# Optimization experiments

Measured on AMD Instinct MI355X. Metric: run time of the kernel, lower is better.

Reference implementation:

```python
import jax, jax.numpy as jnp
import numpy as np

U, M, E, EL, H, F, C = 200000, 100000, 2000000, 500000, 64, 20, 7


def setup_inputs() -> dict:
    key = jax.random.key(0)
    ks = jax.random.split(key, 20)
    s = 0.02
    return {
        "user_node_id": jnp.arange(U, dtype=jnp.int64),
        "movie_node_id": jnp.arange(M, dtype=jnp.int64),
        "movie_x": jax.random.normal(ks[0], (M, F), jnp.float32),
        "edge_src": jax.random.randint(ks[1], (E,), 0, U),
        "edge_dst": jax.random.randint(ks[2], (E,), 0, M),
        "el_src": jax.random.randint(ks[3], (EL,), 0, U),
        "el_dst": jax.random.randint(ks[4], (EL,), 0, M),
        "user_emb": jax.random.normal(ks[5], (U, H), jnp.float32) * s,
        "movie_emb": jax.random.normal(ks[6], (M, H), jnp.float32) * s,
        "w_movie": jax.random.normal(ks[7], (F, H), jnp.float32) * s,
        "b_movie": jnp.zeros((H,), jnp.float32),
        "l1_rates_Wl": jax.random.normal(ks[8], (H, H), jnp.float32) * s,
        "l1_rates_bl": jnp.zeros((H,), jnp.float32),
        "l1_rates_Wr": jax.random.normal(ks[9], (H, H), jnp.float32) * s,
        "l1_rev_Wl": jax.random.normal(ks[10], (H, H), jnp.float32) * s,
        "l1_rev_bl": jnp.zeros((H,), jnp.float32),
        "l1_rev_Wr": jax.random.normal(ks[11], (H, H), jnp.float32) * s,
        "l2_rates_Wl": jax.random.normal(ks[12], (H, H), jnp.float32) * s,
        "l2_rates_bl": jnp.zeros((H,), jnp.float32),
        "l2_rates_Wr": jax.random.normal(ks[13], (H, H), jnp.float32) * s,
        "l2_rev_Wl": jax.random.normal(ks[14], (H, H), jnp.float32) * s,
        "l2_rev_bl": jnp.zeros((H,), jnp.float32),
        "l2_rev_Wr": jax.random.normal(ks[15], (H, H), jnp.float32) * s,
        "cls_W": jax.random.normal(ks[16], (2 * H, C), jnp.float32) * s,
        "cls_b": jnp.zeros((C,), jnp.float32),
    }


def _sage(x_src, x_dst, src, dst, n_dst, Wl, bl, Wr):
    # mean-aggregate neighbor messages: gather -> segment_sum -> divide by degree
    msg = x_src[src]                                            # [E, H]
    agg = jax.ops.segment_sum(msg, dst, num_segments=n_dst)     # [n_dst, H]
    deg = jax.ops.segment_sum(jnp.ones((src.shape[0],), x_src.dtype), dst,
                              num_segments=n_dst)
    agg = agg / jnp.maximum(deg, 1.0)[:, None]
    return agg @ Wl + bl + x_dst @ Wr                           # SAGEConv: lin_l(aggr) + lin_r(root)


def reference(user_node_id, movie_node_id, movie_x, edge_src, edge_dst,
              el_src, el_dst, user_emb, movie_emb, w_movie, b_movie,
              l1_rates_Wl, l1_rates_bl, l1_rates_Wr,
              l1_rev_Wl, l1_rev_bl, l1_rev_Wr,
              l2_rates_Wl, l2_rates_bl, l2_rates_Wr,
              l2_rev_Wl, l2_rev_bl, l2_rev_Wr,
              cls_W, cls_b):
    # input projections
    x_user = user_emb[user_node_id]                              # [U, H]
    x_movie = movie_x @ w_movie + b_movie + movie_emb[movie_node_id]  # [M, H]

    # hetero GNN layer 1 (relu)
    u1 = jax.nn.relu(_sage(x_movie, x_user, edge_dst, edge_src, x_user.shape[0],
                           l1_rev_Wl, l1_rev_bl, l1_rev_Wr))
    m1 = jax.nn.relu(_sage(x_user, x_movie, edge_src, edge_dst, x_movie.shape[0],
                           l1_rates_Wl, l1_rates_bl, l1_rates_Wr))
    # hetero GNN layer 2 (no activation)
    u2 = _sage(m1, u1, edge_dst, edge_src, u1.shape[0],
               l2_rev_Wl, l2_rev_bl, l2_rev_Wr)
    m2 = _sage(u1, m1, edge_src, edge_dst, m1.shape[0],
               l2_rates_Wl, l2_rates_bl, l2_rates_Wr)

    # edge classifier over labeled (user, movie) pairs
    edge_feat = jnp.concatenate([u2[el_src], m2[el_dst]], axis=-1)  # [EL, 2H]
    return edge_feat @ cls_W + cls_b                                # [EL, C]
```

## Files before the change

kernel.cpp:

```cpp
#include <hip/hip_runtime.h>
#include <cstdint>
#include <cstddef>

#define H 64
#define C 7
#define F 20
#define BSH 9
#define BSZ 512
#define CH 8192

typedef unsigned short u16;
typedef __attribute__((ext_vector_type(8))) short bf16x8;
typedef __attribute__((ext_vector_type(4))) float f32x4;
typedef __attribute__((ext_vector_type(2))) float f32x2;

static __device__ __forceinline__ int imax(int a, int b) { return a > b ? a : b; }
static __device__ __forceinline__ int imin(int a, int b) { return a < b ? a : b; }

static __device__ __forceinline__ float bf2f(u16 v) {
  union { unsigned u; float f; } x; x.u = ((unsigned)v) << 16; return x.f;
}
static __device__ __forceinline__ u16 f2bf(float f) {
  union { float f; unsigned u; } x; x.f = f;
  unsigned r = x.u + 0x7fffu + ((x.u >> 16) & 1u);
  return (u16)(r >> 16);
}
static __device__ __forceinline__ int pack2bf(float a, float b) {
  return (int)f2bf(a) | ((int)f2bf(b) << 16);
}
static __device__ __forceinline__ float lo16f(unsigned v) {
  union { unsigned u; float f; } x; x.u = v << 16; return x.f;
}
static __device__ __forceinline__ float hi16f(unsigned v) {
  union { unsigned u; float f; } x; x.u = v & 0xffff0000u; return x.f;
}
static __device__ __forceinline__ int cvtpk_bf16(float a, float b) {
  int w;
  asm("v_cvt_pk_bf16_f32 %0, %1, %2" : "=v"(w) : "v"(a), "v"(b));
  return w;
}

__global__ __launch_bounds__(256) void k_bhist(const int* __restrict__ esrc,
                                               const int* __restrict__ edst, int E,
                                               int* __restrict__ gcnt_u, int* __restrict__ gcnt_m,
                                               int nbu, int nbm) {
  extern __shared__ int sh[];
  int* hu = sh;
  int* hm = sh + nbu;
  for (int i = threadIdx.x; i < nbu + nbm; i += 256) sh[i] = 0;
  __syncthreads();
  int stride = gridDim.x * 256;
  for (int i = blockIdx.x * 256 + threadIdx.x; i < E; i += stride) {
    atomicAdd(&hu[esrc[i] >> BSH], 1);
    atomicAdd(&hm[edst[i] >> BSH], 1);
  }
  __syncthreads();
  for (int i = threadIdx.x; i < nbu; i += 256) if (hu[i]) atomicAdd(&gcnt_u[i], hu[i]);
  for (int i = threadIdx.x; i < nbm; i += 256) if (hm[i]) atomicAdd(&gcnt_m[i], hm[i]);
}

__global__ __launch_bounds__(256) void k_bscan(const int* __restrict__ gcnt_u,
                                               const int* __restrict__ gcnt_m,
                                               int nbu, int nbm, int E,
                                               int* __restrict__ boff_u, int* __restrict__ boff_m,
                                               int* __restrict__ gcur_u, int* __restrict__ gcur_m) {
  __shared__ int s[1024];
  for (int i = threadIdx.x; i < nbu; i += 256) s[i] = gcnt_u[i];
  for (int i = threadIdx.x; i < nbm; i += 256) s[512 + i] = gcnt_m[i];
  __syncthreads();
  if (threadIdx.x == 0) {
    int r = 0;
    for (int i = 0; i < nbu; ++i) { int v = s[i]; s[i] = r; r += v; }
  }
  if (threadIdx.x == 1) {
    int r = 0;
    for (int i = 0; i < nbm; ++i) { int v = s[512 + i]; s[512 + i] = r; r += v; }
  }
  __syncthreads();
  for (int i = threadIdx.x; i < nbu; i += 256) { boff_u[i] = s[i]; gcur_u[i] = s[i]; }
  for (int i = threadIdx.x; i < nbm; i += 256) { boff_m[i] = s[512 + i]; gcur_m[i] = s[512 + i]; }
  if (threadIdx.x == 0) { boff_u[nbu] = E; boff_m[nbm] = E; }
}

__global__ __launch_bounds__(256) void k_bscat(const int* __restrict__ esrc,
                                               const int* __restrict__ edst, int E,
                                               int* __restrict__ gcur_u, int* __restrict__ gcur_m,
                                               unsigned int* __restrict__ pk_u,
                                               unsigned int* __restrict__ pk_m,
                                               int nbu, int nbm, int nchunks) {
  extern __shared__ int sh2[];
  int dir = (blockIdx.x >= (unsigned)nchunks) ? 1 : 0;
  int chunk = dir ? (blockIdx.x - nchunks) : blockIdx.x;
  const int* key = dir ? edst : esrc;
  const int* pay = dir ? esrc : edst;
  int* gcur = dir ? gcur_m : gcur_u;
  unsigned int* pk = dir ? pk_m : pk_u;
  int nb = dir ? nbm : nbu;
  int* cnt = sh2;
  int* base = sh2 + nb;
  int beg = chunk * CH;
  int end = imin(beg + CH, E);
  for (int i = threadIdx.x; i < nb; i += 256) cnt[i] = 0;
  __syncthreads();
  for (int i = beg + threadIdx.x; i < end; i += 256) atomicAdd(&cnt[key[i] >> BSH], 1);
  __syncthreads();
  for (int i = threadIdx.x; i < nb; i += 256) {
    int c = cnt[i];
    base[i] = c ? atomicAdd(&gcur[i], c) : 0;
    cnt[i] = 0;
  }
  __syncthreads();
  for (int i = beg + threadIdx.x; i < end; i += 256) {
    int k = key[i];
    int b = k >> BSH;
    int r = atomicAdd(&cnt[b], 1);
    pk[base[b] + r] = ((unsigned)(k & (BSZ - 1)) << 18) | (unsigned)pay[i];
  }
}

__global__ __launch_bounds__(512) void k_bbuild(const unsigned int* __restrict__ pk_u,
                                                const unsigned int* __restrict__ pk_m,
                                                const int* __restrict__ boff_u,
                                                const int* __restrict__ boff_m,
                                                int nbu, int nbm, int U_, int M_, int E,
                                                int* __restrict__ csr_u, int* __restrict__ csr_m,
                                                int* __restrict__ off_u, int* __restrict__ off_m) {
  __shared__ int hist[BSZ];
  __shared__ int cur[BSZ];
  int dir = (blockIdx.x >= (unsigned)nbu) ? 1 : 0;
  int b = dir ? (blockIdx.x - nbu) : blockIdx.x;
  const unsigned int* pk = dir ? pk_m : pk_u;
  const int* boff = dir ? boff_m : boff_u;
  int N = dir ? M_ : U_;
  int nb = dir ? nbm : nbu;
  int* csr = dir ? csr_m : csr_u;
  int* off = dir ? off_m : off_u;
  int beg = boff[b], end = boff[b + 1];
  int t = threadIdx.x;
  hist[t] = 0;
  __syncthreads();
  for (int i = beg + t; i < end; i += 512) atomicAdd(&hist[pk[i] >> 18], 1);
  __syncthreads();
  int v0 = hist[t];
  for (int o = 1; o < 512; o <<= 1) {
    int x = (t >= o) ? hist[t - o] : 0;
    __syncthreads();
    hist[t] += x;
    __syncthreads();
  }
  int excl = hist[t] - v0;
  cur[t] = excl;
  int node = (b << BSH) + t;
  if (node < N) off[node] = beg + excl;
  if (t == 0 && b == nb - 1) off[N] = E;
  __syncthreads();
  for (int i = beg + t; i < end; i += 512) {
    unsigned int p = pk[i];
    int n = (int)(p >> 18);
    int r = atomicAdd(&cur[n], 1);
    csr[beg + r] = (int)(p & 0x3FFFFu);
  }
}

__global__ __launch_bounds__(256) void k_prep(
    const float* __restrict__ movie_x, const float* __restrict__ w_movie,
    const float* __restrict__ b_movie, const float* __restrict__ movie_emb,
    const int* __restrict__ mnid,
    const float* __restrict__ user_emb, const int* __restrict__ unid,
    const float* __restrict__ l2u_Wl, const float* __restrict__ l2u_Wr,
    const float* __restrict__ l2u_bl,
    const float* __restrict__ l2m_Wl, const float* __restrict__ l2m_Wr,
    const float* __restrict__ l2m_bl,
    const float* __restrict__ clsW,
    u16* __restrict__ xm_bf, u16* __restrict__ xu_bf, float* __restrict__ cw,
    int M_, int U_, int gProj, int gCvt) {
  __shared__ float ws_[F * H];
  int b = blockIdx.x;
  if (b < gProj) {
    for (int i = threadIdx.x; i < F * H; i += 256) ws_[i] = w_movie[i];
    __syncthreads();
    int t = b * 256 + threadIdx.x;
    int m = t >> 6;
    int h = t & 63;
    if (m >= M_) return;
    float acc = b_movie[h] + movie_emb[(size_t)mnid[m] * H + h];
    const float* xr = movie_x + (size_t)m * F;
    #pragma unroll
    for (int f = 0; f < F; ++f) acc += xr[f] * ws_[f * H + h];
    xm_bf[(size_t)m * H + h] = f2bf(acc);
  } else if (b < gProj + gCvt) {
    int t = (b - gProj) * 256 + threadIdx.x;
    if (t >= U_ * 16) return;
    int i = t >> 4;
    int g = t & 15;
    const float4 v = *(const float4*)(user_emb + (size_t)unid[i] * H + g * 4);
    ushort4 o;
    o.x = f2bf(v.x); o.y = f2bf(v.y); o.z = f2bf(v.z); o.w = f2bf(v.w);
    *(ushort4*)(xu_bf + (size_t)i * H + g * 4) = o;
  } else {
    int t = (b - gProj - gCvt) * 256 + threadIdx.x;
    if (t < 448) {
      int k = t / C, c = t % C;
      float s = 0.f;
      for (int j = 0; j < H; ++j) s += l2u_Wl[k * H + j] * clsW[j * C + c];
      cw[t] = s;
    } else if (t < 896) {
      int u = t - 448; int k = u / C, c = u % C;
      float s = 0.f;
      for (int j = 0; j < H; ++j) s += l2u_Wr[k * H + j] * clsW[j * C + c];
      cw[t] = s;
    } else if (t < 1344) {
      int u = t - 896; int k = u / C, c = u % C;
      float s = 0.f;
      for (int j = 0; j < H; ++j) s += l2m_Wl[k * H + j] * clsW[(H + j) * C + c];
      cw[t] = s;
    } else if (t < 1792) {
      int u = t - 1344; int k = u / C, c = u % C;
      float s = 0.f;
      for (int j = 0; j < H; ++j) s += l2m_Wr[k * H + j] * clsW[(H + j) * C + c];
      cw[t] = s;
    } else if (t < 1799) {
      int c = t - 1792;
      float s = 0.f;
      for (int j = 0; j < H; ++j) s += l2u_bl[j] * clsW[j * C + c];
      cw[t] = s;
    } else if (t < 1806) {
      int c = t - 1799;
      float s = 0.f;
      for (int j = 0; j < H; ++j) s += l2m_bl[j] * clsW[(H + j) * C + c];
      cw[t] = s;
    } else if (t < 1870) {
      xm_bf[(size_t)M_ * H + (t - 1806)] = 0;
    } else if (t < 1934) {
      xu_bf[(size_t)U_ * H + (t - 1870)] = 0;
    }
  }
}

__global__ __launch_bounds__(512, 4) void k_sage_mfma(
    const u16* __restrict__ xu, const u16* __restrict__ xm,
    const int* __restrict__ csr_u, const int* __restrict__ off_u,
    const int* __restrict__ csr_m, const int* __restrict__ off_m,
    const float* __restrict__ WlU, const float* __restrict__ blU, const float* __restrict__ WrU,
    const float* __restrict__ WlM, const float* __restrict__ blM, const float* __restrict__ WrM,
    const float* __restrict__ CWml, const float* __restrict__ CWur,
    const float* __restrict__ CWul, const float* __restrict__ CWmr,
    u16* __restrict__ Zu, u16* __restrict__ Zm,
    int U_, int M_, int E_, int gU) {
  __shared__ int sWl[64 * 36];
  __shared__ int sWr[64 * 36];
  __shared__ int sAggHi[128 * 36];
  __shared__ int sAggLo[128 * 36];
  __shared__ int sCC[16 * 36];
  __shared__ float sBl[64];

  int movie = (blockIdx.x >= (unsigned)gU) ? 1 : 0;
  int bside = movie ? (blockIdx.x - gU) : blockIdx.x;
  const u16* srcT = movie ? xu : xm;
  const u16* rootT = movie ? xm : xu;
  const int* csr = movie ? csr_m : csr_u;
  const int* off = movie ? off_m : off_u;
  const float* Wl = movie ? WlM : WlU;
  const float* Wr = movie ? WrM : WrU;
  const float* bl = movie ? blM : blU;
  const float* CWl = movie ? CWul : CWml;
  const float* CWr = movie ? CWmr : CWur;
  u16* Z = movie ? Zm : Zu;
  int N = movie ? M_ : U_;
  int zrow = movie ? U_ : M_;

  int tid = threadIdx.x;
  for (int idx = tid; idx < 2048; idx += 512) {
    int j = idx & 63, kk = idx >> 6;
    sWl[j * 36 + kk] = pack2bf(Wl[(2 * kk) * H + j], Wl[(2 * kk + 1) * H + j]);
    sWr[j * 36 + kk] = pack2bf(Wr[(2 * kk) * H + j], Wr[(2 * kk + 1) * H + j]);
  }
  for (int idx = tid; idx < 512; idx += 512) {
    int cc = idx >> 5, kk = idx & 31;
    float f0, f1;
    if (cc < 7)       { f0 = CWl[(2 * kk) * C + cc];     f1 = CWl[(2 * kk + 1) * C + cc]; }
    else if (cc == 7) { f0 = 0.f; f1 = 0.f; }
    else if (cc < 15) { f0 = CWr[(2 * kk) * C + cc - 8]; f1 = CWr[(2 * kk + 1) * C + cc - 8]; }
    else              { f0 = 0.f; f1 = 0.f; }
    sCC[cc * 36 + kk] = pack2bf(f0, f1);
  }
  if (tid < 64) sBl[tid] = bl[tid];
  __syncthreads();

  int lane = tid & 63;
  int wid = tid >> 6;
  int slot = lane >> 3;
  int l3 = lane & 7;
  int sbase = slot * 8;
  int node0 = bside * 128 + wid * 16;

  #pragma unroll
  for (int g = 0; g < 2; ++g) {
    int n = node0 + g * 8 + slot;
    int nc = n < N ? n : N - 1;
    int jb = off[nc];
    int d = off[nc + 1] - jb;
    if (n >= N) d = 0;
    int dmax = d;
    dmax = imax(dmax, __shfl_xor(dmax, 8));
    dmax = imax(dmax, __shfl_xor(dmax, 16));
    dmax = imax(dmax, __shfl_xor(dmax, 32));

    f32x2 acc2[4] = {{0.f, 0.f}, {0.f, 0.f}, {0.f, 0.f}, {0.f, 0.f}};
    for (int tb = 0; tb < dmax; tb += 8) {
      int idx = tb + l3;
      int ci = imin(jb + idx, E_ - 1);
      int e = (idx < d) ? csr[ci] : zrow;
      uint4 v[8];
      #pragma unroll
      for (int k = 0; k < 8; ++k) {
        int a = __shfl(e, sbase + k);
        v[k] = *(const uint4*)(srcT + (size_t)(unsigned)a * H + l3 * 8);
      }
      #pragma unroll
      for (int k = 0; k < 8; ++k) {
        f32x2 p0 = {lo16f(v[k].x), hi16f(v[k].x)};
        f32x2 p1 = {lo16f(v[k].y), hi16f(v[k].y)};
        f32x2 p2 = {lo16f(v[k].z), hi16f(v[k].z)};
        f32x2 p3 = {lo16f(v[k].w), hi16f(v[k].w)};
        acc2[0] += p0; acc2[1] += p1; acc2[2] += p2; acc2[3] += p3;
      }
    }

    float inv = 1.0f / (float)imax(d, 1);
    int hi4[4], lo4[4];
    #pragma unroll
    for (int pp = 0; pp < 4; ++pp) {
      float s0 = acc2[pp].x * inv;
      float s1 = acc2[pp].y * inv;
      int w = cvtpk_bf16(s0, s1);
      float r0 = s0 - lo16f((unsigned)w);
      float r1 = s1 - hi16f((unsigned)w);
      hi4[pp] = w;
      lo4[pp] = cvtpk_bf16(r0, r1);
    }
    int row = wid * 16 + g * 8 + slot;
    *(int4*)&sAggHi[row * 36 + l3 * 4] = *(int4*)hi4;
    *(int4*)&sAggLo[row * 36 + l3 * 4] = *(int4*)lo4;
  }

  int r16 = lane & 15;
  int q4 = lane >> 4;
  union FU { int4 i; bf16x8 b; };
  FU ahi[2], alo[2], art[2];
  int arow = wid * 16 + r16;
  int rnode = node0 + r16;
  rnode = rnode < N ? rnode : N - 1;
  #pragma unroll
  for (int kt = 0; kt < 2; ++kt) {
    ahi[kt].i = *(const int4*)&sAggHi[arow * 36 + kt * 16 + q4 * 4];
    alo[kt].i = *(const int4*)&sAggLo[arow * 36 + kt * 16 + q4 * 4];
    art[kt].i = ((const int4*)(rootT + (size_t)rnode * H))[kt * 4 + q4];
  }

  u16* sVT = (u16*)(sAggHi + (size_t)wid * 16 * 36);
  const int* sVTd = sAggHi + (size_t)wid * 16 * 36;

  #pragma unroll
  for (int t = 0; t < 4; ++t) {
    f32x4 cacc = {0.f, 0.f, 0.f, 0.f};
    #pragma unroll
    for (int kt = 0; kt < 2; ++kt) {
      FU bwl, bwr;
      bwl.i = *(const int4*)&sWl[(t * 16 + r16) * 36 + kt * 16 + q4 * 4];
      bwr.i = *(const int4*)&sWr[(t * 16 + r16) * 36 + kt * 16 + q4 * 4];
      cacc = __builtin_amdgcn_mfma_f32_16x16x32_bf16(ahi[kt].b, bwl.b, cacc, 0, 0, 0);
      cacc = __builtin_amdgcn_mfma_f32_16x16x32_bf16(alo[kt].b, bwl.b, cacc, 0, 0, 0);
      cacc = __builtin_amdgcn_mfma_f32_16x16x32_bf16(art[kt].b, bwr.b, cacc, 0, 0, 0);
    }
    float bj = sBl[t * 16 + r16];
    float v0 = fmaxf(cacc[0] + bj, 0.f);
    float v1 = fmaxf(cacc[1] + bj, 0.f);
    float v2 = fmaxf(cacc[2] + bj, 0.f);
    float v3 = fmaxf(cacc[3] + bj, 0.f);
    int w01 = cvtpk_bf16(v0, v1);
    int w23 = cvtpk_bf16(v2, v3);
    int base = (q4 * 4) * 72 + t * 16 + r16;
    sVT[base]       = (u16)w01;
    sVT[base + 72]  = (u16)((unsigned)w01 >> 16);
    sVT[base + 144] = (u16)w23;
    sVT[base + 216] = (u16)((unsigned)w23 >> 16);
  }

  f32x4 z4 = {0.f, 0.f, 0.f, 0.f};
  #pragma unroll
  for (int kt = 0; kt < 2; ++kt) {
    FU a2, b2;
    a2.i = *(const int4*)&sVTd[r16 * 36 + kt * 16 + q4 * 4];
    b2.i = *(const int4*)&sCC[r16 * 36 + kt * 16 + q4 * 4];
    z4 = __builtin_amdgcn_mfma_f32_16x16x32_bf16(a2.b, b2.b, z4, 0, 0, 0);
  }
  #pragma unroll
  for (int r = 0; r < 4; ++r) {
    int node = node0 + q4 * 4 + r;
    if (node < N) Z[(size_t)node * 16 + r16] = f2bf(z4[r]);
  }
}

__global__ __launch_bounds__(256) void k_agg7m(
    const u16* __restrict__ Zu, const u16* __restrict__ Zm,
    const int* __restrict__ csr_u, const int* __restrict__ off_u,
    const int* __restrict__ csr_m, const int* __restrict__ off_m,
    const float* __restrict__ cbu, const float* __restrict__ cbm,
    float* __restrict__ Pu, float* __restrict__ Pm,
    int U_, int M_, int gU) {
  int movie = (blockIdx.x >= (unsigned)gU) ? 1 : 0;
  int bside = movie ? (blockIdx.x - gU) : blockIdx.x;
  const u16* Zsrc = movie ? Zu : Zm;
  const u16* Zroot = movie ? Zm : Zu;
  const int* csr = movie ? csr_m : csr_u;
  const int* off = movie ? off_m : off_u;
  const float* cb = movie ? cbm : cbu;
  float* P = movie ? Pm : Pu;
  int N = movie ? M_ : U_;

  int n = bside * 256 + threadIdx.x;
  if (n >= N) return;
  int beg = off[n], end = off[n + 1];
  float acc[8] = {0.f, 0.f, 0.f, 0.f, 0.f, 0.f, 0.f, 0.f};
  for (int j = beg; j < end; ++j) {
    int a = csr[j];
    uint4 z = *(const uint4*)(Zsrc + (size_t)a * 16);
    acc[0] += lo16f(z.x); acc[1] += hi16f(z.x);
    acc[2] += lo16f(z.y); acc[3] += hi16f(z.y);
    acc[4] += lo16f(z.z); acc[5] += hi16f(z.z);
    acc[6] += lo16f(z.w); acc[7] += hi16f(z.w);
  }
  float inv = 1.f / (float)imax(end - beg, 1);
  uint4 zr = *(const uint4*)(Zroot + (size_t)n * 16 + 8);
  float4 o0, o1;
  o0.x = acc[0] * inv + lo16f(zr.x) + cb[0];
  o0.y = acc[1] * inv + hi16f(zr.x) + cb[1];
  o0.z = acc[2] * inv + lo16f(zr.y) + cb[2];
  o0.w = acc[3] * inv + hi16f(zr.y) + cb[3];
  o1.x = acc[4] * inv + lo16f(zr.z) + cb[4];
  o1.y = acc[5] * inv + hi16f(zr.z) + cb[5];
  o1.z = acc[6] * inv + lo16f(zr.w) + cb[6];
  o1.w = 0.f;
  float4* po = (float4*)(P + (size_t)n * 8);
  po[0] = o0;
  po[1] = o1;
}

__global__ void k_final(const int* __restrict__ els, const int* __restrict__ eld,
                        const float* __restrict__ Pu, const float* __restrict__ Pm,
                        const float* __restrict__ clsb, float* __restrict__ out, int total) {
  int t = blockIdx.x * 256 + threadIdx.x;
  if (t >= total) return;
  int e = t / C, c = t - e * C;
  out[t] = Pu[(size_t)els[e] * 8 + c] + Pm[(size_t)eld[e] * 8 + c] + clsb[c];
}

extern "C" void kernel_launch(void* const* d_in, const int* in_sizes, int n_in,
                              void* d_out, int out_size, void* d_ws, size_t ws_size,
                              hipStream_t stream) {
  (void)n_in; (void)out_size; (void)ws_size;
  const int*   unid      = (const int*)d_in[0];
  const int*   mnid      = (const int*)d_in[1];
  const float* movie_x   = (const float*)d_in[2];
  const int*   e_src     = (const int*)d_in[3];
  const int*   e_dst     = (const int*)d_in[4];
  const int*   el_src    = (const int*)d_in[5];
  const int*   el_dst    = (const int*)d_in[6];
  const float* user_emb  = (const float*)d_in[7];
  const float* movie_emb = (const float*)d_in[8];
  const float* w_movie   = (const float*)d_in[9];
  const float* b_movie   = (const float*)d_in[10];
  const float* l1r_Wl    = (const float*)d_in[11];
  const float* l1r_bl    = (const float*)d_in[12];
  const float* l1r_Wr    = (const float*)d_in[13];
  const float* l1v_Wl    = (const float*)d_in[14];
  const float* l1v_bl    = (const float*)d_in[15];
  const float* l1v_Wr    = (const float*)d_in[16];
  const float* l2r_Wl    = (const float*)d_in[17];
  const float* l2r_bl    = (const float*)d_in[18];
  const float* l2r_Wr    = (const float*)d_in[19];
  const float* l2v_Wl    = (const float*)d_in[20];
  const float* l2v_bl    = (const float*)d_in[21];
  const float* l2v_Wr    = (const float*)d_in[22];
  const float* cls_W     = (const float*)d_in[23];
  const float* cls_b     = (const float*)d_in[24];

  int U  = in_sizes[0];
  int M  = in_sizes[1];
  int E  = in_sizes[3];
  int EL = in_sizes[5];

  int nbu = (U + BSZ - 1) / BSZ;
  int nbm = (M + BSZ - 1) / BSZ;
  int nchunks = (E + CH - 1) / CH;

  char* p = (char*)d_ws;
  auto alloc = [&](size_t nbytes) { char* r = p; p += (nbytes + 255) & ~(size_t)255; return r; };

  u16*   xm_bf  = (u16*)alloc((size_t)(M + 1) * H * 2);
  u16*   xu_bf  = (u16*)alloc((size_t)(U + 1) * H * 2);
  u16*   Zu     = (u16*)alloc((size_t)U * 16 * 2);
  u16*   Zm     = (u16*)alloc((size_t)M * 16 * 2);
  float* Pu     = (float*)alloc((size_t)U * 8 * 4);
  float* Pm     = (float*)alloc((size_t)M * 8 * 4);
  int*   csr_u  = (int*)alloc((size_t)E * 4);
  int*   csr_m  = (int*)alloc((size_t)E * 4);
  int*   off_u  = (int*)alloc((size_t)(U + 1) * 4);
  int*   off_m  = (int*)alloc((size_t)(M + 1) * 4);
  unsigned int* pk_u = (unsigned int*)alloc((size_t)E * 4);
  unsigned int* pk_m = (unsigned int*)alloc((size_t)E * 4);
  int*   gcnt   = (int*)alloc((size_t)(nbu + nbm) * 4);
  int*   gcnt_u = gcnt;
  int*   gcnt_m = gcnt + nbu;
  int*   boff_u = (int*)alloc((size_t)(nbu + 1) * 4);
  int*   boff_m = (int*)alloc((size_t)(nbm + 1) * 4);
  int*   gcur_u = (int*)alloc((size_t)nbu * 4);
  int*   gcur_m = (int*)alloc((size_t)nbm * 4);
  float* cw     = (float*)alloc(1806 * 4);
  float* CWul = cw, *CWur = cw + 448, *CWml = cw + 896, *CWmr = cw + 1344;
  float* cbu  = cw + 1792, *cbm = cw + 1799;

  hipMemsetAsync(gcnt, 0, (size_t)(nbu + nbm) * 4, stream);

  k_bhist<<<256, 256, (size_t)(nbu + nbm) * 4, stream>>>(e_src, e_dst, E, gcnt_u, gcnt_m, nbu, nbm);
  k_bscan<<<1, 256, 0, stream>>>(gcnt_u, gcnt_m, nbu, nbm, E, boff_u, boff_m, gcur_u, gcur_m);
  k_bscat<<<2 * nchunks, 256, (size_t)(2 * nbu) * 4, stream>>>(e_src, e_dst, E, gcur_u, gcur_m,
                                                               pk_u, pk_m, nbu, nbm, nchunks);
  k_bbuild<<<nbu + nbm, 512, 0, stream>>>(pk_u, pk_m, boff_u, boff_m, nbu, nbm, U, M, E,
                                          csr_u, csr_m, off_u, off_m);

  int gProj = (M * H + 255) / 256;
  int gCvt  = (U * 16 + 255) / 256;
  k_prep<<<gProj + gCvt + 8, 256, 0, stream>>>(
      movie_x, w_movie, b_movie, movie_emb, mnid, user_emb, unid,
      l2v_Wl, l2v_Wr, l2v_bl, l2r_Wl, l2r_Wr, l2r_bl, cls_W,
      xm_bf, xu_bf, cw, M, U, gProj, gCvt);

  int gU_s = (U + 127) / 128;
  int gM_s = (M + 127) / 128;
  k_sage_mfma<<<gU_s + gM_s, 512, 0, stream>>>(
      xu_bf, xm_bf, csr_u, off_u, csr_m, off_m,
      l1v_Wl, l1v_bl, l1v_Wr,
      l1r_Wl, l1r_bl, l1r_Wr,
      CWml, CWur, CWul, CWmr,
      Zu, Zm, U, M, E, gU_s);

  int gU_a = (U + 255) / 256;
  int gM_a = (M + 255) / 256;
  k_agg7m<<<gU_a + gM_a, 256, 0, stream>>>(Zu, Zm, csr_u, off_u, csr_m, off_m,
                                           cbu, cbm, Pu, Pm, U, M, gU_a);

  int total = EL * C;
  k_final<<<(total + 255) / 256, 256, 0, stream>>>(el_src, el_dst, Pu, Pm, cls_b, (float*)d_out, total);
}
```

Before: 500.9 us.

## Split Z into aggregate/root planes, shrink LDS, unroll agg gather

The per-node Z output is split into separate 8-wide arrays: the aggregated half (gathered by neighbors) and the root half (read once per node). This halves the bytes each gather row fetches in the second aggregation, and that loop is unrolled by four to keep more loads in flight. LDS use in the sage kernel is cut: Wl and Wr are merged into one padded buffer, the lo-aggregate buffer uses a tighter stride, and the classifier weights and bias now live in registers. Launch bounds are raised to 6 blocks per CU to raise occupancy, which risks register pressure or spills.

```diff
diff --git a/kernel.cpp b/kernel.cpp
--- a/kernel.cpp
+++ b/kernel.cpp
@@ -237,7 +237,7 @@
   }
 }
 
-__global__ __launch_bounds__(512, 4) void k_sage_mfma(
+__global__ __launch_bounds__(512, 6) void k_sage_mfma(
     const u16* __restrict__ xu, const u16* __restrict__ xm,
     const int* __restrict__ csr_u, const int* __restrict__ off_u,
     const int* __restrict__ csr_m, const int* __restrict__ off_m,
@@ -245,14 +245,12 @@
     const float* __restrict__ WlM, const float* __restrict__ blM, const float* __restrict__ WrM,
     const float* __restrict__ CWml, const float* __restrict__ CWur,
     const float* __restrict__ CWul, const float* __restrict__ CWmr,
-    u16* __restrict__ Zu, u16* __restrict__ Zm,
+    u16* __restrict__ Zau, u16* __restrict__ Zru,
+    u16* __restrict__ Zam, u16* __restrict__ Zrm,
     int U_, int M_, int E_, int gU) {
-  __shared__ int sWl[64 * 36];
-  __shared__ int sWr[64 * 36];
+  __shared__ int sWlr[64 * 68];
   __shared__ int sAggHi[128 * 36];
-  __shared__ int sAggLo[128 * 36];
-  __shared__ int sCC[16 * 36];
-  __shared__ float sBl[64];
+  __shared__ int sAggLo[128 * 34];
 
   int movie = (blockIdx.x >= (unsigned)gU) ? 1 : 0;
   int bside = movie ? (blockIdx.x - gU) : blockIdx.x;
@@ -265,34 +263,54 @@
   const float* bl = movie ? blM : blU;
   const float* CWl = movie ? CWul : CWml;
   const float* CWr = movie ? CWmr : CWur;
-  u16* Z = movie ? Zm : Zu;
+  u16* Za = movie ? Zam : Zau;
+  u16* Zr = movie ? Zrm : Zru;
   int N = movie ? M_ : U_;
   int zrow = movie ? U_ : M_;
 
   int tid = threadIdx.x;
+  int lane = tid & 63;
+  int wid = tid >> 6;
+  int r16 = lane & 15;
+  int q4 = lane >> 4;
+  int node0 = bside * 128 + wid * 16;
+
+  union FU { int4 i; bf16x8 b; int w[4]; };
+
+  float bj4[4];
+  #pragma unroll
+  for (int t = 0; t < 4; ++t) bj4[t] = bl[t * 16 + r16];
+  int rnode = node0 + r16;
+  rnode = rnode < N ? rnode : N - 1;
+  FU art[2];
+  #pragma unroll
+  for (int kt = 0; kt < 2; ++kt)
+    art[kt].i = ((const int4*)(rootT + (size_t)rnode * H))[kt * 4 + q4];
+  FU ccf[2];
+  #pragma unroll
+  for (int kt = 0; kt < 2; ++kt) {
+    #pragma unroll
+    for (int i = 0; i < 4; ++i) {
+      int kk = kt * 16 + q4 * 4 + i;
+      float f0, f1;
+      if (r16 < 7)       { f0 = CWl[(2 * kk) * C + r16];     f1 = CWl[(2 * kk + 1) * C + r16]; }
+      else if (r16 == 7) { f0 = 0.f; f1 = 0.f; }
+      else if (r16 < 15) { f0 = CWr[(2 * kk) * C + r16 - 8]; f1 = CWr[(2 * kk + 1) * C + r16 - 8]; }
+      else               { f0 = 0.f; f1 = 0.f; }
+      ccf[kt].w[i] = pack2bf(f0, f1);
+    }
+  }
+
   for (int idx = tid; idx < 2048; idx += 512) {
     int j = idx & 63, kk = idx >> 6;
-    sWl[j * 36 + kk] = pack2bf(Wl[(2 * kk) * H + j], Wl[(2 * kk + 1) * H + j]);
-    sWr[j * 36 + kk] = pack2bf(Wr[(2 * kk) * H + j], Wr[(2 * kk + 1) * H + j]);
-  }
-  for (int idx = tid; idx < 512; idx += 512) {
-    int cc = idx >> 5, kk = idx & 31;
-    float f0, f1;
-    if (cc < 7)       { f0 = CWl[(2 * kk) * C + cc];     f1 = CWl[(2 * kk + 1) * C + cc]; }
-    else if (cc == 7) { f0 = 0.f; f1 = 0.f; }
-    else if (cc < 15) { f0 = CWr[(2 * kk) * C + cc - 8]; f1 = CWr[(2 * kk + 1) * C + cc - 8]; }
-    else              { f0 = 0.f; f1 = 0.f; }
-    sCC[cc * 36 + kk] = pack2bf(f0, f1);
-  }
-  if (tid < 64) sBl[tid] = bl[tid];
-  __syncthreads();
-
-  int lane = tid & 63;
-  int wid = tid >> 6;
+    sWlr[j * 68 + kk]      = pack2bf(Wl[(2 * kk) * H + j], Wl[(2 * kk + 1) * H + j]);
+    sWlr[j * 68 + 32 + kk] = pack2bf(Wr[(2 * kk) * H + j], Wr[(2 * kk + 1) * H + j]);
+  }
+  __syncthreads();
+
   int slot = lane >> 3;
   int l3 = lane & 7;
   int sbase = slot * 8;
-  int node0 = bside * 128 + wid * 16;
 
   #pragma unroll
   for (int g = 0; g < 2; ++g) {
@@ -341,21 +359,18 @@
     }
     int row = wid * 16 + g * 8 + slot;
     *(int4*)&sAggHi[row * 36 + l3 * 4] = *(int4*)hi4;
-    *(int4*)&sAggLo[row * 36 + l3 * 4] = *(int4*)lo4;
-  }
-
-  int r16 = lane & 15;
-  int q4 = lane >> 4;
-  union FU { int4 i; bf16x8 b; };
-  FU ahi[2], alo[2], art[2];
+    *(int2*)&sAggLo[row * 34 + l3 * 4]     = *(int2*)&lo4[0];
+    *(int2*)&sAggLo[row * 34 + l3 * 4 + 2] = *(int2*)&lo4[2];
+  }
+
+  FU ahi[2], alo[2];
   int arow = wid * 16 + r16;
-  int rnode = node0 + r16;
-  rnode = rnode < N ? rnode : N - 1;
   #pragma unroll
   for (int kt = 0; kt < 2; ++kt) {
     ahi[kt].i = *(const int4*)&sAggHi[arow * 36 + kt * 16 + q4 * 4];
-    alo[kt].i = *(const int4*)&sAggLo[arow * 36 + kt * 16 + q4 * 4];
-    art[kt].i = ((const int4*)(rootT + (size_t)rnode * H))[kt * 4 + q4];
+    int2 l0 = *(const int2*)&sAggLo[arow * 34 + kt * 16 + q4 * 4];
+    int2 l1 = *(const int2*)&sAggLo[arow * 34 + kt * 16 + q4 * 4 + 2];
+    alo[kt].w[0] = l0.x; alo[kt].w[1] = l0.y; alo[kt].w[2] = l1.x; alo[kt].w[3] = l1.y;
   }
 
   u16* sVT = (u16*)(sAggHi + (size_t)wid * 16 * 36);
@@ -367,13 +382,13 @@
     #pragma unroll
     for (int kt = 0; kt < 2; ++kt) {
       FU bwl, bwr;
-      bwl.i = *(const int4*)&sWl[(t * 16 + r16) * 36 + kt * 16 + q4 * 4];
-      bwr.i = *(const int4*)&sWr[(t * 16 + r16) * 36 + kt * 16 + q4 * 4];
+      bwl.i = *(const int4*)&sWlr[(t * 16 + r16) * 68 + kt * 16 + q4 * 4];
+      bwr.i = *(const int4*)&sWlr[(t * 16 + r16) * 68 + 32 + kt * 16 + q4 * 4];
       cacc = __builtin_amdgcn_mfma_f32_16x16x32_bf16(ahi[kt].b, bwl.b, cacc, 0, 0, 0);
       cacc = __builtin_amdgcn_mfma_f32_16x16x32_bf16(alo[kt].b, bwl.b, cacc, 0, 0, 0);
       cacc = __builtin_amdgcn_mfma_f32_16x16x32_bf16(art[kt].b, bwr.b, cacc, 0, 0, 0);
     }
-    float bj = sBl[t * 16 + r16];
+    float bj = bj4[t];
     float v0 = fmaxf(cacc[0] + bj, 0.f);
     float v1 = fmaxf(cacc[1] + bj, 0.f);
     float v2 = fmaxf(cacc[2] + bj, 0.f);
@@ -390,20 +405,29 @@
   f32x4 z4 = {0.f, 0.f, 0.f, 0.f};
   #pragma unroll
   for (int kt = 0; kt < 2; ++kt) {
-    FU a2, b2;
+    FU a2;
     a2.i = *(const int4*)&sVTd[r16 * 36 + kt * 16 + q4 * 4];
-    b2.i = *(const int4*)&sCC[r16 * 36 + kt * 16 + q4 * 4];
-    z4 = __builtin_amdgcn_mfma_f32_16x16x32_bf16(a2.b, b2.b, z4, 0, 0, 0);
-  }
+    z4 = __builtin_amdgcn_mfma_f32_16x16x32_bf16(a2.b, ccf[kt].b, z4, 0, 0, 0);
+  }
+  u16* Zp = (r16 < 8) ? Za : Zr;
+  int col = r16 & 7;
   #pragma unroll
   for (int r = 0; r < 4; ++r) {
     int node = node0 + q4 * 4 + r;
-    if (node < N) Z[(size_t)node * 16 + r16] = f2bf(z4[r]);
-  }
+    if (node < N) Zp[(size_t)node * 8 + col] = f2bf(z4[r]);
+  }
+}
+
+static __device__ __forceinline__ void accz8(float* acc, uint4 zv) {
+  acc[0] += lo16f(zv.x); acc[1] += hi16f(zv.x);
+  acc[2] += lo16f(zv.y); acc[3] += hi16f(zv.y);
+  acc[4] += lo16f(zv.z); acc[5] += hi16f(zv.z);
+  acc[6] += lo16f(zv.w); acc[7] += hi16f(zv.w);
 }
 
 __global__ __launch_bounds__(256) void k_agg7m(
-    const u16* __restrict__ Zu, const u16* __restrict__ Zm,
+    const u16* __restrict__ Zau, const u16* __restrict__ Zru,
+    const u16* __restrict__ Zam, const u16* __restrict__ Zrm,
     const int* __restrict__ csr_u, const int* __restrict__ off_u,
     const int* __restrict__ csr_m, const int* __restrict__ off_m,
     const float* __restrict__ cbu, const float* __restrict__ cbm,
@@ -411,8 +435,8 @@
     int U_, int M_, int gU) {
   int movie = (blockIdx.x >= (unsigned)gU) ? 1 : 0;
   int bside = movie ? (blockIdx.x - gU) : blockIdx.x;
-  const u16* Zsrc = movie ? Zu : Zm;
-  const u16* Zroot = movie ? Zm : Zu;
+  const u16* Zsrc = movie ? Zau : Zam;
+  const u16* Zroot = movie ? Zrm : Zru;
   const int* csr = movie ? csr_m : csr_u;
   const int* off = movie ? off_m : off_u;
   const float* cb = movie ? cbm : cbu;
@@ -423,16 +447,21 @@
   if (n >= N) return;
   int beg = off[n], end = off[n + 1];
   float acc[8] = {0.f, 0.f, 0.f, 0.f, 0.f, 0.f, 0.f, 0.f};
-  for (int j = beg; j < end; ++j) {
-    int a = csr[j];
-    uint4 z = *(const uint4*)(Zsrc + (size_t)a * 16);
-    acc[0] += lo16f(z.x); acc[1] += hi16f(z.x);
-    acc[2] += lo16f(z.y); acc[3] += hi16f(z.y);
-    acc[4] += lo16f(z.z); acc[5] += hi16f(z.z);
-    acc[6] += lo16f(z.w); acc[7] += hi16f(z.w);
+  int j = beg;
+  for (; j + 4 <= end; j += 4) {
+    int a0 = csr[j], a1 = csr[j + 1], a2 = csr[j + 2], a3 = csr[j + 3];
+    uint4 z0 = *(const uint4*)(Zsrc + (size_t)a0 * 8);
+    uint4 z1 = *(const uint4*)(Zsrc + (size_t)a1 * 8);
+    uint4 z2 = *(const uint4*)(Zsrc + (size_t)a2 * 8);
+    uint4 z3 = *(const uint4*)(Zsrc + (size_t)a3 * 8);
+    accz8(acc, z0); accz8(acc, z1); accz8(acc, z2); accz8(acc, z3);
+  }
+  for (; j < end; ++j) {
+    uint4 zv = *(const uint4*)(Zsrc + (size_t)csr[j] * 8);
+    accz8(acc, zv);
   }
   float inv = 1.f / (float)imax(end - beg, 1);
-  uint4 zr = *(const uint4*)(Zroot + (size_t)n * 16 + 8);
+  uint4 zr = *(const uint4*)(Zroot + (size_t)n * 8);
   float4 o0, o1;
   o0.x = acc[0] * inv + lo16f(zr.x) + cb[0];
   o0.y = acc[1] * inv + hi16f(zr.x) + cb[1];
@@ -500,8 +529,10 @@
 
   u16*   xm_bf  = (u16*)alloc((size_t)(M + 1) * H * 2);
   u16*   xu_bf  = (u16*)alloc((size_t)(U + 1) * H * 2);
-  u16*   Zu     = (u16*)alloc((size_t)U * 16 * 2);
-  u16*   Zm     = (u16*)alloc((size_t)M * 16 * 2);
+  u16*   Zau    = (u16*)alloc((size_t)U * 8 * 2);
+  u16*   Zru    = (u16*)alloc((size_t)U * 8 * 2);
+  u16*   Zam    = (u16*)alloc((size_t)M * 8 * 2);
+  u16*   Zrm    = (u16*)alloc((size_t)M * 8 * 2);
   float* Pu     = (float*)alloc((size_t)U * 8 * 4);
   float* Pm     = (float*)alloc((size_t)M * 8 * 4);
   int*   csr_u  = (int*)alloc((size_t)E * 4);
@@ -544,11 +575,11 @@
       l1v_Wl, l1v_bl, l1v_Wr,
       l1r_Wl, l1r_bl, l1r_Wr,
       CWml, CWur, CWul, CWmr,
-      Zu, Zm, U, M, E, gU_s);
+      Zau, Zru, Zam, Zrm, U, M, E, gU_s);
 
   int gU_a = (U + 255) / 256;
   int gM_a = (M + 255) / 256;
-  k_agg7m<<<gU_a + gM_a, 256, 0, stream>>>(Zu, Zm, csr_u, off_u, csr_m, off_m,
+  k_agg7m<<<gU_a + gM_a, 256, 0, stream>>>(Zau, Zru, Zam, Zrm, csr_u, off_u, csr_m, off_m,
                                            cbu, cbm, Pu, Pm, U, M, gU_a);
 
   int total = EL * C;
```

After: 486.2 us. -2.9%, faster.
